# Performance work log

Hardware: AMD Instinct MI355X
Metric: run time of the kernel (lower is better)

The kernel has to match this reference:

```python
import jax, jax.numpy as jnp
import numpy as np

LATENT = 512
MEL = 80


def _lstm(x, Wk, Wr, b):
    # x: [B, T, Din]; Keras gate order i, f, g(cell), o
    B = x.shape[0]
    D = Wr.shape[0]
    h0 = jnp.zeros((B, D), x.dtype)
    c0 = jnp.zeros((B, D), x.dtype)

    def step(carry, xt):
        h, c = carry
        z = xt @ Wk + h @ Wr + b  # [B, 4D]
        i, f, g, o = jnp.split(z, 4, axis=-1)
        i = jax.nn.sigmoid(i)
        f = jax.nn.sigmoid(f)
        g = jnp.tanh(g)
        o = jax.nn.sigmoid(o)
        c = f * c + i * g
        h = o * jnp.tanh(c)
        return (h, c), h

    (h_f, c_f), hs = jax.lax.scan(step, (h0, c0), x.transpose(1, 0, 2))
    return hs.transpose(1, 0, 2), h_f, c_f  # [B,T,D], [B,D], [B,D]


def setup_inputs() -> dict:
    key = jax.random.key(0)
    ks = jax.random.split(key, 10)
    B, Td, Te, Din, D = 8, 256, 256, MEL, LATENT
    s = lambda k, shp, fan: jax.random.normal(k, shp, jnp.float32) / np.sqrt(fan)
    return {
        "inputs": jax.random.normal(ks[0], (B, Td, Din), jnp.float32),
        "attended_inputs": jax.random.normal(ks[1], (B, Te, D), jnp.float32),
        "lstm_Wk": s(ks[2], (Din, 4 * D), Din),
        "lstm_Wr": s(ks[3], (D, 4 * D), D),
        "lstm_b": jnp.zeros((4 * D,), jnp.float32),
        "W1": s(ks[4], (D, D), D),
        "b1": jnp.zeros((D,), jnp.float32),
        "W3": s(ks[5], (D, 1), D),
        "b3": jnp.zeros((1,), jnp.float32),
        "Wout": s(ks[6], (2 * D, MEL), 2 * D),
        "bout": jnp.zeros((MEL,), jnp.float32),
    }


def reference(inputs, attended_inputs, lstm_Wk, lstm_Wr, lstm_b, W1, b1, W3, b3, Wout, bout):
    x, state_h, state_c = _lstm(inputs, lstm_Wk, lstm_Wr, lstm_b)  # [B,Td,D]
    # NOTE: original code uses dense1 for BOTH projections (dense2 unused)
    half1 = (attended_inputs @ W1 + b1)[:, None, :, :]   # [B,1,Te,D]
    half2 = (x @ W1 + b1)[:, :, None, :]                 # [B,Td,1,D]
    scores = jnp.squeeze(jnp.tanh(half1 + half2) @ W3 + b3, -1)  # [B,Td,Te]
    attn = jax.nn.softmax(scores, axis=-1)
    weighted = jnp.einsum('bde,bef->bdf', attn, attended_inputs)  # [B,Td,D]
    x = jnp.concatenate([x, weighted], axis=2)           # [B,Td,2D]
    out = x @ Wout + bout                                 # [B,Td,MEL]
    return out, state_h, state_c
```

## Files before the change

### kernel.cpp

```cpp
#include <hip/hip_runtime.h>
#include <cstdint>
#include <cmath>

#define TD 256
#define TE 256
#define NB 8
#define DD 512
#define DIN 80
#define NMEL 80

typedef unsigned long long u64;

__global__ __launch_bounds__(256) void gemm_bias_k(const float* __restrict__ A,
    const float* __restrict__ B, const float* __restrict__ bias,
    float* __restrict__ C, int M, int N, int K)
{
    __shared__ float As[64][17];
    __shared__ __align__(16) float Bs[16][64];
    const int tid = threadIdx.x;
    const int tx = tid & 15, ty = tid >> 4;
    const int n0 = blockIdx.x * 64, m0 = blockIdx.y * 64;
    float acc[4][4] = {};
    for (int k0 = 0; k0 < K; k0 += 16) {
#pragma unroll
        for (int i = 0; i < 4; ++i) {
            int lin = tid + i * 256;
            int k = lin & 15, m = lin >> 4;
            As[m][k] = A[(size_t)(m0 + m) * K + k0 + k];
        }
#pragma unroll
        for (int i = 0; i < 4; ++i) {
            int lin = tid + i * 256;
            int n = lin & 63, k = lin >> 6;
            Bs[k][n] = B[(size_t)(k0 + k) * N + n0 + n];
        }
        __syncthreads();
#pragma unroll
        for (int kk = 0; kk < 16; ++kk) {
            float a0 = As[ty * 4 + 0][kk], a1 = As[ty * 4 + 1][kk];
            float a2 = As[ty * 4 + 2][kk], a3 = As[ty * 4 + 3][kk];
            const float4 b4 = *(const float4*)&Bs[kk][tx * 4];
            acc[0][0] += a0 * b4.x; acc[0][1] += a0 * b4.y; acc[0][2] += a0 * b4.z; acc[0][3] += a0 * b4.w;
            acc[1][0] += a1 * b4.x; acc[1][1] += a1 * b4.y; acc[1][2] += a1 * b4.z; acc[1][3] += a1 * b4.w;
            acc[2][0] += a2 * b4.x; acc[2][1] += a2 * b4.y; acc[2][2] += a2 * b4.z; acc[2][3] += a2 * b4.w;
            acc[3][0] += a3 * b4.x; acc[3][1] += a3 * b4.y; acc[3][2] += a3 * b4.z; acc[3][3] += a3 * b4.w;
        }
        __syncthreads();
    }
    const float4 bv = *(const float4*)&bias[n0 + tx * 4];
#pragma unroll
    for (int i = 0; i < 4; ++i) {
        float4 o;
        o.x = acc[i][0] + bv.x; o.y = acc[i][1] + bv.y;
        o.z = acc[i][2] + bv.z; o.w = acc[i][3] + bv.w;
        *(float4*)&C[(size_t)(m0 + ty * 4 + i) * N + n0 + tx * 4] = o;
    }
}

__global__ __launch_bounds__(256, 1) void lstm_k(const float* __restrict__ Zx,
    const float* __restrict__ Wr, float* __restrict__ hs,
    u64* __restrict__ hpub,
    float* __restrict__ outh, float* __restrict__ outc)
{
    __shared__ __align__(16) float h_s[512];
    __shared__ float part[256];
    const int b = blockIdx.x & 7;
    const int g = blockIdx.x >> 3;
    const int tid = threadIdx.x;
    const int wv = tid >> 6;
    const int lane = tid & 63;
    const int gcol = ((lane >> 4) << 9) | (g << 4) | (lane & 15);
    const int col = (g << 4) | (lane & 15);

    float w[128];
    {
        const float* wb = Wr + (size_t)(wv * 128) * 2048 + gcol;
#pragma unroll
        for (int i = 0; i < 128; ++i) w[i] = wb[(size_t)i * 2048];
    }
    float creg = 0.f, hlast = 0.f;
    u64* const pub0 = hpub + (size_t)b * 512;
    u64* const pub1 = hpub + (size_t)(8 + b) * 512;

    for (int t = 0; t < TD; ++t) {
        float zx = 0.f;
        if (wv == 0) zx = Zx[(size_t)(b * TD + t) * 2048 + gcol];

        {
            u64* const pr = (t & 1) ? pub1 : pub0;
            const unsigned stag = (unsigned)t;
            u64 v0 = 0, v1 = 0;
            bool d0 = false, d1 = false;
            for (;;) {
                if (!d0) { v0 = __hip_atomic_load(pr + tid, __ATOMIC_RELAXED, __HIP_MEMORY_SCOPE_AGENT);
                           d0 = ((unsigned)(v0 >> 32) == stag); }
                if (!d1) { v1 = __hip_atomic_load(pr + tid + 256, __ATOMIC_RELAXED, __HIP_MEMORY_SCOPE_AGENT);
                           d1 = ((unsigned)(v1 >> 32) == stag); }
                if (d0 && d1) break;
                __builtin_amdgcn_s_sleep(1);
            }
            h_s[tid]       = __uint_as_float((unsigned)v0);
            h_s[tid + 256] = __uint_as_float((unsigned)v1);
        }
        __syncthreads();

        float acc = 0.f;
        {
            const float4* h4 = (const float4*)(h_s + (wv << 7));
#pragma unroll
            for (int i = 0; i < 32; ++i) {
                float4 h = h4[i];
                acc += w[4 * i + 0] * h.x;
                acc += w[4 * i + 1] * h.y;
                acc += w[4 * i + 2] * h.z;
                acc += w[4 * i + 3] * h.w;
            }
        }
        part[tid] = acc;
        __syncthreads();
        if (wv == 0) {
            float z = part[lane] + part[64 + lane] + part[128 + lane] + part[192 + lane] + zx;
            float zf = __shfl(z, lane + 16);
            float zg = __shfl(z, lane + 32);
            float zo = __shfl(z, lane + 48);
            if (lane < 16) {
                float ig = 1.f / (1.f + expf(-z));
                float fg = 1.f / (1.f + expf(-zf));
                float gg = tanhf(zg);
                float og = 1.f / (1.f + expf(-zo));
                creg = fg * creg + ig * gg;
                hlast = og * tanhf(creg);
                u64 pv = ((u64)(unsigned)(t + 1) << 32) | (u64)__float_as_uint(hlast);
                u64* const pw = (t & 1) ? pub0 : pub1;
                __hip_atomic_store(pw + col, pv, __ATOMIC_RELAXED, __HIP_MEMORY_SCOPE_AGENT);
                hs[(size_t)(b * TD + t) * 512 + col] = hlast;
            }
        }
    }
    if (wv == 0 && lane < 16) {
        outh[b * 512 + col] = hlast;
        outc[b * 512 + col] = creg;
    }
}

__global__ __launch_bounds__(256) void attn_k(const float* __restrict__ half1,
    const float* __restrict__ half2, const float* __restrict__ att,
    const float* __restrict__ W3, const float* __restrict__ b3,
    float* __restrict__ wgt)
{
    __shared__ __align__(16) float h2s[4][512];
    __shared__ __align__(16) float sc[4][256];
    __shared__ __align__(16) float av[8][512];
    const int tid = threadIdx.x;
    const int bb = blockIdx.x >> 6;
    const int d0 = (blockIdx.x & 63) * 4;
    const float C2 = 2.885390081777927f;

#pragma unroll
    for (int i = 0; i < 8; ++i) {
        int lin = tid + i * 256;
        int r = lin >> 9, k = lin & 511;
        h2s[r][k] = half2[(size_t)(bb * TD + d0 + r) * 512 + k] * C2;
    }
    __syncthreads();
    {
        const float* h1p = half1 + (size_t)(bb * TE + tid) * 512;
        float accs[4] = {0.f, 0.f, 0.f, 0.f};
        for (int k = 0; k < 512; k += 4) {
            float4 h1 = *(const float4*)(h1p + k);
            float4 w3 = *(const float4*)(W3 + k);
            float u0 = h1.x * C2, u1 = h1.y * C2, u2 = h1.z * C2, u3 = h1.w * C2;
#pragma unroll
            for (int r = 0; r < 4; ++r) {
                float t0 = 1.f - 2.f * __builtin_amdgcn_rcpf(__builtin_amdgcn_exp2f(u0 + h2s[r][k + 0]) + 1.f);
                float t1 = 1.f - 2.f * __builtin_amdgcn_rcpf(__builtin_amdgcn_exp2f(u1 + h2s[r][k + 1]) + 1.f);
                float t2 = 1.f - 2.f * __builtin_amdgcn_rcpf(__builtin_amdgcn_exp2f(u2 + h2s[r][k + 2]) + 1.f);
                float t3 = 1.f - 2.f * __builtin_amdgcn_rcpf(__builtin_amdgcn_exp2f(u3 + h2s[r][k + 3]) + 1.f);
                accs[r] += t0 * w3.x + t1 * w3.y + t2 * w3.z + t3 * w3.w;
            }
        }
        const float b3v = b3[0];
#pragma unroll
        for (int r = 0; r < 4; ++r) sc[r][tid] = accs[r] + b3v;
    }
    __syncthreads();
    {
        const int r = tid >> 6, l = tid & 63;
        float4 v = *(const float4*)&sc[r][l * 4];
        float mx = fmaxf(fmaxf(v.x, v.y), fmaxf(v.z, v.w));
#pragma unroll
        for (int off = 32; off; off >>= 1) mx = fmaxf(mx, __shfl_xor(mx, off));
        const float L2E = 1.44269504089f;
        float e0 = __builtin_amdgcn_exp2f((v.x - mx) * L2E);
        float e1 = __builtin_amdgcn_exp2f((v.y - mx) * L2E);
        float e2 = __builtin_amdgcn_exp2f((v.z - mx) * L2E);
        float e3 = __builtin_amdgcn_exp2f((v.w - mx) * L2E);
        float s = e0 + e1 + e2 + e3;
#pragma unroll
        for (int off = 32; off; off >>= 1) s += __shfl_xor(s, off);
        float inv = 1.f / s;
        float4 p; p.x = e0 * inv; p.y = e1 * inv; p.z = e2 * inv; p.w = e3 * inv;
        *(float4*)&sc[r][l * 4] = p;
    }
    __syncthreads();
    float acc[4][2] = {};
    for (int e0 = 0; e0 < TE; e0 += 8) {
#pragma unroll
        for (int i = 0; i < 16; ++i) {
            int lin = tid + i * 256;
            int e = lin >> 9, k = lin & 511;
            av[e][k] = att[(size_t)(bb * TE + e0 + e) * 512 + k];
        }
        __syncthreads();
#pragma unroll
        for (int ee = 0; ee < 8; ++ee) {
            float x0 = av[ee][tid], x1 = av[ee][tid + 256];
#pragma unroll
            for (int r = 0; r < 4; ++r) {
                float p = sc[r][e0 + ee];
                acc[r][0] += p * x0;
                acc[r][1] += p * x1;
            }
        }
        __syncthreads();
    }
#pragma unroll
    for (int r = 0; r < 4; ++r) {
        wgt[(size_t)(bb * TD + d0 + r) * 512 + tid] = acc[r][0];
        wgt[(size_t)(bb * TD + d0 + r) * 512 + tid + 256] = acc[r][1];
    }
}

__global__ __launch_bounds__(256) void outgemm_k(const float* __restrict__ x,
    const float* __restrict__ wgt, const float* __restrict__ Wout,
    const float* __restrict__ bout, float* __restrict__ out)
{
    __shared__ float As[64][17];
    __shared__ float Bs[16][80];
    const int tid = threadIdx.x;
    const int tx = tid & 15, ty = tid >> 4;
    const int m0 = blockIdx.x * 64;
    const int ks = blockIdx.y;
    float acc[4][5] = {};
    for (int kt = 0; kt < 16; ++kt) {
        const int k0 = ks * 256 + kt * 16;
        const float* src = (k0 < 512) ? x : wgt;
        const int kk0 = (k0 < 512) ? k0 : (k0 - 512);
#pragma unroll
        for (int i = 0; i < 4; ++i) {
            int lin = tid + i * 256;
            int k = lin & 15, m = lin >> 4;
            As[m][k] = src[(size_t)(m0 + m) * 512 + kk0 + k];
        }
#pragma unroll
        for (int i = 0; i < 5; ++i) {
            int lin = tid + i * 256;
            int n = lin % 80, k = lin / 80;
            Bs[k][n] = Wout[(size_t)(k0 + k) * 80 + n];
        }
        __syncthreads();
#pragma unroll
        for (int kk = 0; kk < 16; ++kk) {
            float a[4], bv[5];
#pragma unroll
            for (int i = 0; i < 4; ++i) a[i] = As[ty * 4 + i][kk];
#pragma unroll
            for (int j = 0; j < 5; ++j) bv[j] = Bs[kk][tx * 5 + j];
#pragma unroll
            for (int i = 0; i < 4; ++i)
#pragma unroll
                for (int j = 0; j < 5; ++j) acc[i][j] += a[i] * bv[j];
        }
        __syncthreads();
    }
#pragma unroll
    for (int i = 0; i < 4; ++i) {
#pragma unroll
        for (int j = 0; j < 5; ++j) {
            float v = acc[i][j];
            if (ks == 0) v += bout[tx * 5 + j];
            atomicAdd(&out[(size_t)(m0 + ty * 4 + i) * 80 + tx * 5 + j], v);
        }
    }
}

extern "C" void kernel_launch(void* const* d_in, const int* in_sizes, int n_in,
                              void* d_out, int out_size, void* d_ws, size_t ws_size,
                              hipStream_t stream)
{
    (void)in_sizes; (void)n_in; (void)out_size; (void)ws_size;
    const float* inputs = (const float*)d_in[0];
    const float* att    = (const float*)d_in[1];
    const float* Wk     = (const float*)d_in[2];
    const float* Wr     = (const float*)d_in[3];
    const float* lb     = (const float*)d_in[4];
    const float* W1     = (const float*)d_in[5];
    const float* b1     = (const float*)d_in[6];
    const float* W3     = (const float*)d_in[7];
    const float* b3     = (const float*)d_in[8];
    const float* Wout   = (const float*)d_in[9];
    const float* bout   = (const float*)d_in[10];

    float* out  = (float*)d_out;
    float* outh = out + 2048 * 80;
    float* outc = outh + 8 * 512;

    char* ws = (char*)d_ws;
    float* Zx    = (float*)(ws);
    float* half1 = (float*)(ws + (16u << 20));
    float* half2 = (float*)(ws + (20u << 20));
    float* hsx   = (float*)(ws + (24u << 20));
    float* wgt   = (float*)(ws + (28u << 20));
    u64*   hpub  = (u64*)(ws + (32u << 20));

    (void)hipMemsetAsync(ws + (32u << 20), 0, 2 * 8 * 512 * sizeof(u64), stream);
    (void)hipMemsetAsync(d_out, 0, (size_t)2048 * 80 * 4, stream);

    gemm_bias_k<<<dim3(32, 32), 256, 0, stream>>>(inputs, Wk, lb, Zx, 2048, 2048, 80);
    gemm_bias_k<<<dim3(8, 32), 256, 0, stream>>>(att, W1, b1, half1, 2048, 512, 512);

    void* args[] = { (void*)&Zx, (void*)&Wr, (void*)&hsx, (void*)&hpub,
                     (void*)&outh, (void*)&outc };
    (void)hipLaunchCooperativeKernel((void*)lstm_k, dim3(256), dim3(256), args, 0, stream);

    gemm_bias_k<<<dim3(8, 32), 256, 0, stream>>>(hsx, W1, b1, half2, 2048, 512, 512);
    attn_k<<<dim3(512), 256, 0, stream>>>(half1, half2, att, W3, b3, wgt);
    outgemm_k<<<dim3(32, 4), 256, 0, stream>>>(hsx, wgt, Wout, bout, out);
}
```

Measured before the change: 929.4 us.

## Restructure LSTM step to reduce within-wave, remove second barrier, use fast exp/rcp

Each wave now owns four hidden columns across all four gates, with the K dimension split over 16-lane quarters of the wave. The partial dot products are reduced with cross-lane shuffles instead of a shared-memory exchange, which removes the second __syncthreads per timestep. The h vector is double-buffered in padded shared memory so the next step's writes don't race with the current step's reads. Sigmoid and tanh now use hardware exp2/rcp intrinsics, trading a little accuracy for a shorter latency-bound serial chain.

New measurement: 1.011 ms. 8.8% more time.

```diff
diff --git a/kernel.cpp b/kernel.cpp
--- a/kernel.cpp
+++ b/kernel.cpp
@@ -62,19 +62,27 @@
     u64* __restrict__ hpub,
     float* __restrict__ outh, float* __restrict__ outc)
 {
-    __shared__ __align__(16) float h_s[512];
-    __shared__ float part[256];
+    __shared__ __align__(16) float h_s[2][544];
     const int b = blockIdx.x & 7;
     const int g = blockIdx.x >> 3;
     const int tid = threadIdx.x;
     const int wv = tid >> 6;
     const int lane = tid & 63;
-    const int gcol = ((lane >> 4) << 9) | (g << 4) | (lane & 15);
-    const int col = (g << 4) | (lane & 15);
+    const int kq = lane >> 4;
+    const int idx = lane & 15;
+    const int gate = idx >> 2;
+    const int hoff = idx & 3;
+    const int hcol = (g << 4) | (wv << 2) | hoff;
+    const int gcol = (gate << 9) | hcol;
+    const float L2E = 1.442695040888963f;
+    const bool isG = (gate == 2);
+    const float mscale = isG ? (-2.f * L2E) : (-L2E);
+    const float aA = isG ? 2.f : 1.f;
+    const float aB = isG ? -1.f : 0.f;
 
     float w[128];
     {
-        const float* wb = Wr + (size_t)(wv * 128) * 2048 + gcol;
+        const float* wb = Wr + (size_t)(kq * 128) * 2048 + gcol;
 #pragma unroll
         for (int i = 0; i < 128; ++i) w[i] = wb[(size_t)i * 2048];
     }
@@ -83,8 +91,7 @@
     u64* const pub1 = hpub + (size_t)(8 + b) * 512;
 
     for (int t = 0; t < TD; ++t) {
-        float zx = 0.f;
-        if (wv == 0) zx = Zx[(size_t)(b * TD + t) * 2048 + gcol];
+        float zx = Zx[(size_t)(b * TD + t) * 2048 + gcol];
 
         {
             u64* const pr = (t & 1) ? pub1 : pub0;
@@ -99,14 +106,16 @@
                 if (d0 && d1) break;
                 __builtin_amdgcn_s_sleep(1);
             }
-            h_s[tid]       = __uint_as_float((unsigned)v0);
-            h_s[tid + 256] = __uint_as_float((unsigned)v1);
+            float* hb = h_s[t & 1];
+            const int j0 = tid, j1 = tid + 256;
+            hb[(j0 >> 7) * 136 + (j0 & 127)] = __uint_as_float((unsigned)v0);
+            hb[(j1 >> 7) * 136 + (j1 & 127)] = __uint_as_float((unsigned)v1);
         }
         __syncthreads();
 
         float acc = 0.f;
         {
-            const float4* h4 = (const float4*)(h_s + (wv << 7));
+            const float4* h4 = (const float4*)(h_s[t & 1] + kq * 136);
 #pragma unroll
             for (int i = 0; i < 32; ++i) {
                 float4 h = h4[i];
@@ -116,30 +125,31 @@
                 acc += w[4 * i + 3] * h.w;
             }
         }
-        part[tid] = acc;
-        __syncthreads();
-        if (wv == 0) {
-            float z = part[lane] + part[64 + lane] + part[128 + lane] + part[192 + lane] + zx;
-            float zf = __shfl(z, lane + 16);
-            float zg = __shfl(z, lane + 32);
-            float zo = __shfl(z, lane + 48);
-            if (lane < 16) {
-                float ig = 1.f / (1.f + expf(-z));
-                float fg = 1.f / (1.f + expf(-zf));
-                float gg = tanhf(zg);
-                float og = 1.f / (1.f + expf(-zo));
-                creg = fg * creg + ig * gg;
-                hlast = og * tanhf(creg);
-                u64 pv = ((u64)(unsigned)(t + 1) << 32) | (u64)__float_as_uint(hlast);
-                u64* const pw = (t & 1) ? pub0 : pub1;
-                __hip_atomic_store(pw + col, pv, __ATOMIC_RELAXED, __HIP_MEMORY_SCOPE_AGENT);
-                hs[(size_t)(b * TD + t) * 512 + col] = hlast;
-            }
-        }
-    }
-    if (wv == 0 && lane < 16) {
-        outh[b * 512 + col] = hlast;
-        outc[b * 512 + col] = creg;
+        acc += __shfl_xor(acc, 16);
+        acc += __shfl_xor(acc, 32);
+        float z = acc + zx;
+        float e = __builtin_amdgcn_exp2f(z * mscale);
+        float s = __builtin_amdgcn_rcpf(1.f + e);
+        float act = fmaf(s, aA, aB);
+        const int basel = (lane & 48) | hoff;
+        float ii = __shfl(act, basel);
+        float ff = __shfl(act, basel | 4);
+        float gg = __shfl(act, basel | 8);
+        float oo = __shfl(act, basel | 12);
+        if (lane < 4) {
+            creg = fmaf(ff, creg, ii * gg);
+            float e2 = __builtin_amdgcn_exp2f(creg * (-2.f * L2E));
+            float th = fmaf(2.f, __builtin_amdgcn_rcpf(1.f + e2), -1.f);
+            hlast = oo * th;
+            u64 pv = ((u64)(unsigned)(t + 1) << 32) | (u64)__float_as_uint(hlast);
+            u64* const pw = (t & 1) ? pub0 : pub1;
+            __hip_atomic_store(pw + hcol, pv, __ATOMIC_RELAXED, __HIP_MEMORY_SCOPE_AGENT);
+            hs[(size_t)(b * TD + t) * 512 + hcol] = hlast;
+        }
+    }
+    if (lane < 4) {
+        outh[b * 512 + hcol] = hlast;
+        outc[b * 512 + hcol] = creg;
     }
 }
 
```

## Fuse pre-LSTM GEMMs into one launch and stage half1 through LDS in attention

Applied to the files above, without the earlier changes.

The two independent input GEMMs (input projection and attended projection) now run in a single launch, with the block index deciding which one a block computes, so one kernel launch is saved. In the attention kernel, each thread used to stream its own half1 row with strided float4 loads. Now 32-column chunks of half1 are loaded cooperatively into padded shared memory, which coalesces the global reads. The cost is extra shared memory (about 33 KB), which may lower occupancy, plus added syncthreads per chunk.

Measured after the change: 912.1 us. Within noise of the previous version (-1.9%).

```diff
diff --git a/kernel.cpp b/kernel.cpp
--- a/kernel.cpp
+++ b/kernel.cpp
@@ -11,15 +11,14 @@
 
 typedef unsigned long long u64;
 
-__global__ __launch_bounds__(256) void gemm_bias_k(const float* __restrict__ A,
+__device__ __forceinline__ void gemm_body(const float* __restrict__ A,
     const float* __restrict__ B, const float* __restrict__ bias,
-    float* __restrict__ C, int M, int N, int K)
+    float* __restrict__ C, int N, int K, int m0, int n0)
 {
     __shared__ float As[64][17];
     __shared__ __align__(16) float Bs[16][64];
     const int tid = threadIdx.x;
     const int tx = tid & 15, ty = tid >> 4;
-    const int n0 = blockIdx.x * 64, m0 = blockIdx.y * 64;
     float acc[4][4] = {};
     for (int k0 = 0; k0 < K; k0 += 16) {
 #pragma unroll
@@ -54,6 +53,28 @@
         o.x = acc[i][0] + bv.x; o.y = acc[i][1] + bv.y;
         o.z = acc[i][2] + bv.z; o.w = acc[i][3] + bv.w;
         *(float4*)&C[(size_t)(m0 + ty * 4 + i) * N + n0 + tx * 4] = o;
+    }
+}
+
+__global__ __launch_bounds__(256) void gemm_bias_k(const float* __restrict__ A,
+    const float* __restrict__ B, const float* __restrict__ bias,
+    float* __restrict__ C, int N, int K)
+{
+    gemm_body(A, B, bias, C, N, K, blockIdx.y * 64, blockIdx.x * 64);
+}
+
+__global__ __launch_bounds__(256) void fused_pre_k(
+    const float* __restrict__ inputs, const float* __restrict__ Wk,
+    const float* __restrict__ lb, float* __restrict__ Zx,
+    const float* __restrict__ att, const float* __restrict__ W1,
+    const float* __restrict__ b1, float* __restrict__ half1)
+{
+    int wg = blockIdx.x;
+    if (wg < 1024) {
+        gemm_body(inputs, Wk, lb, Zx, 2048, 80, (wg >> 5) * 64, (wg & 31) * 64);
+    } else {
+        wg -= 1024;
+        gemm_body(att, W1, b1, half1, 512, 512, (wg >> 3) * 64, (wg & 7) * 64);
     }
 }
 
@@ -149,6 +170,7 @@
     float* __restrict__ wgt)
 {
     __shared__ __align__(16) float h2s[4][512];
+    __shared__ float h1s[256 * 33];
     __shared__ __align__(16) float sc[4][256];
     __shared__ __align__(16) float av[8][512];
     const int tid = threadIdx.x;
@@ -162,23 +184,30 @@
         int r = lin >> 9, k = lin & 511;
         h2s[r][k] = half2[(size_t)(bb * TD + d0 + r) * 512 + k] * C2;
     }
-    __syncthreads();
+
+    float accs[4] = {0.f, 0.f, 0.f, 0.f};
+    for (int kc = 0; kc < 512; kc += 32) {
+#pragma unroll
+        for (int i = 0; i < 32; ++i) {
+            int lin = tid + i * 256;
+            int e = lin >> 5, kk = lin & 31;
+            h1s[e * 33 + kk] = half1[(size_t)(bb * TE + e) * 512 + kc + kk] * C2;
+        }
+        __syncthreads();
+        const float* myh1 = h1s + tid * 33;
+#pragma unroll 8
+        for (int kk = 0; kk < 32; ++kk) {
+            float u = myh1[kk];
+            float w = W3[kc + kk];
+#pragma unroll
+            for (int r = 0; r < 4; ++r) {
+                float t = 1.f - 2.f * __builtin_amdgcn_rcpf(__builtin_amdgcn_exp2f(u + h2s[r][kc + kk]) + 1.f);
+                accs[r] += t * w;
+            }
+        }
+        __syncthreads();
+    }
     {
-        const float* h1p = half1 + (size_t)(bb * TE + tid) * 512;
-        float accs[4] = {0.f, 0.f, 0.f, 0.f};
-        for (int k = 0; k < 512; k += 4) {
-            float4 h1 = *(const float4*)(h1p + k);
-            float4 w3 = *(const float4*)(W3 + k);
-            float u0 = h1.x * C2, u1 = h1.y * C2, u2 = h1.z * C2, u3 = h1.w * C2;
-#pragma unroll
-            for (int r = 0; r < 4; ++r) {
-                float t0 = 1.f - 2.f * __builtin_amdgcn_rcpf(__builtin_amdgcn_exp2f(u0 + h2s[r][k + 0]) + 1.f);
-                float t1 = 1.f - 2.f * __builtin_amdgcn_rcpf(__builtin_amdgcn_exp2f(u1 + h2s[r][k + 1]) + 1.f);
-                float t2 = 1.f - 2.f * __builtin_amdgcn_rcpf(__builtin_amdgcn_exp2f(u2 + h2s[r][k + 2]) + 1.f);
-                float t3 = 1.f - 2.f * __builtin_amdgcn_rcpf(__builtin_amdgcn_exp2f(u3 + h2s[r][k + 3]) + 1.f);
-                accs[r] += t0 * w3.x + t1 * w3.y + t2 * w3.z + t3 * w3.w;
-            }
-        }
         const float b3v = b3[0];
 #pragma unroll
         for (int r = 0; r < 4; ++r) sc[r][tid] = accs[r] + b3v;
@@ -316,14 +345,13 @@
     (void)hipMemsetAsync(ws + (32u << 20), 0, 2 * 8 * 512 * sizeof(u64), stream);
     (void)hipMemsetAsync(d_out, 0, (size_t)2048 * 80 * 4, stream);
 
-    gemm_bias_k<<<dim3(32, 32), 256, 0, stream>>>(inputs, Wk, lb, Zx, 2048, 2048, 80);
-    gemm_bias_k<<<dim3(8, 32), 256, 0, stream>>>(att, W1, b1, half1, 2048, 512, 512);
+    fused_pre_k<<<dim3(1280), 256, 0, stream>>>(inputs, Wk, lb, Zx, att, W1, b1, half1);
 
     void* args[] = { (void*)&Zx, (void*)&Wr, (void*)&hsx, (void*)&hpub,
                      (void*)&outh, (void*)&outc };
     (void)hipLaunchCooperativeKernel((void*)lstm_k, dim3(256), dim3(256), args, 0, stream);
 
-    gemm_bias_k<<<dim3(8, 32), 256, 0, stream>>>(hsx, W1, b1, half2, 2048, 512, 512);
+    gemm_bias_k<<<dim3(8, 32), 256, 0, stream>>>(hsx, W1, b1, half2, 512, 512);
     attn_k<<<dim3(512), 256, 0, stream>>>(half1, half2, att, W3, b3, wgt);
     outgemm_k<<<dim3(32, 4), 256, 0, stream>>>(hsx, wgt, Wout, bout, out);
 }
```
